# Performance work log

Hardware: AMD Instinct MI355X
Metric: run time of the kernel (lower is better)

The kernel has to match this reference:

```python
import jax, jax.numpy as jnp
import numpy as np

N_NODES = 40000
N_EDGES = 640000
N_FEAT = 128
HIDDEN = 128
N_GRAPHS = 64


def _sage_conv(x, src, dst, Wl, b, Wr):
    # PyG SAGEConv (aggr='mean', root_weight=True, normalize=False):
    # out_i = W_l @ mean_{j in N(i)} x_j + b + W_r @ x_i
    msg = x[src]                                             # [E, F]
    s = jax.ops.segment_sum(msg, dst, num_segments=N_NODES)  # [N, F]
    deg = jax.ops.segment_sum(jnp.ones((src.shape[0],), x.dtype), dst,
                              num_segments=N_NODES)
    agg = s / jnp.maximum(deg, 1.0)[:, None]
    return agg @ Wl + b + x @ Wr


def setup_inputs() -> dict:
    key = jax.random.key(0)
    ks = jax.random.split(key, 12)
    sc = 1.0 / np.sqrt(N_FEAT)
    x = jax.random.normal(ks[0], (N_NODES, N_FEAT), dtype=jnp.float32)
    edge_index = jax.random.randint(ks[1], (2, N_EDGES), 0, N_NODES, dtype=jnp.int32)
    batch = jnp.sort(jax.random.randint(ks[2], (N_NODES,), 0, N_GRAPHS, dtype=jnp.int32))
    mk = lambda k, shp: (jax.random.normal(k, shp, dtype=jnp.float32) * sc)
    return {
        'x': x, 'edge_index': edge_index, 'batch': batch,
        'W1l': mk(ks[3], (N_FEAT, HIDDEN)), 'b1': jnp.zeros((HIDDEN,), jnp.float32),
        'W1r': mk(ks[4], (N_FEAT, HIDDEN)),
        'W2l': mk(ks[5], (HIDDEN, HIDDEN)), 'b2': jnp.zeros((HIDDEN,), jnp.float32),
        'W2r': mk(ks[6], (HIDDEN, HIDDEN)),
        'W3l': mk(ks[7], (HIDDEN, HIDDEN)), 'b3': jnp.zeros((HIDDEN,), jnp.float32),
        'W3r': mk(ks[8], (HIDDEN, HIDDEN)),
        'Wlin': mk(ks[9], (3 * HIDDEN, HIDDEN)), 'blin': jnp.zeros((HIDDEN,), jnp.float32),
    }


def reference(x, edge_index, batch, W1l, b1, W1r, W2l, b2, W2r, W3l, b3, W3r, Wlin, blin):
    src, dst = edge_index[0], edge_index[1]
    h1 = jax.nn.relu(_sage_conv(x, src, dst, W1l, b1, W1r))
    h2 = jax.nn.relu(_sage_conv(h1, src, dst, W2l, b2, W2r))
    h3 = jax.nn.relu(_sage_conv(h2, src, dst, W3l, b3, W3r))
    h = jnp.concatenate([h1, h2, h3], axis=1)                # [N, 3*H]
    pooled = jax.ops.segment_sum(h, batch, num_segments=N_GRAPHS)  # global_add_pool
    out = jax.nn.relu(pooled @ Wlin + blin)                  # [G, H]
    return out
```

## Files before the change

### kernel.cpp

```cpp
#include <hip/hip_runtime.h>
#include <hip/hip_bf16.h>

#define N_NODES 40000
#define N_EDGES 640000
#define NFEAT 128
#define NGRAPHS 64
#define ECAP 768

typedef __attribute__((ext_vector_type(8))) short short8;
typedef __attribute__((ext_vector_type(4))) float float4v;

static __device__ __forceinline__ float bf2f(unsigned short u) {
    unsigned int x = ((unsigned int)u) << 16;
    return __builtin_bit_cast(float, x);
}
static __device__ __forceinline__ unsigned short f2bf(float f) {
    unsigned int x = __builtin_bit_cast(unsigned int, f);
    unsigned int r = x + 0x7fffu + ((x >> 16) & 1u);
    return (unsigned short)(r >> 16);
}

__global__ void k_prep(const int* __restrict__ dst, int* __restrict__ deg,
                       const int* __restrict__ batch, int* __restrict__ goff,
                       const float* __restrict__ x, unsigned short* __restrict__ h0,
                       const float* __restrict__ Wl0, const float* __restrict__ Wr0,
                       const float* __restrict__ Wl1, const float* __restrict__ Wr1,
                       const float* __restrict__ Wl2, const float* __restrict__ Wr2,
                       unsigned short* __restrict__ Wt, float* __restrict__ pooled) {
    int b = blockIdx.x;
    if (b < 2500) {
        int e = b * 256 + threadIdx.x;
        if (e < N_EDGES) atomicAdd(&deg[dst[e]], 1);
    } else if (b < 2657) {
        int i = (b - 2500) * 256 + threadIdx.x;
        if (i >= N_NODES) return;
        int b1 = batch[i];
        int b0 = (i == 0) ? -1 : batch[i - 1];
        for (int g = b0 + 1; g <= b1; ++g) goff[g] = i;
        if (i == N_NODES - 1)
            for (int g = b1 + 1; g <= NGRAPHS; ++g) goff[g] = N_NODES;
    } else if (b < 5157) {
        int i = (b - 2657) * 256 + threadIdx.x;
        const int n = N_NODES * NFEAT / 8;
        if (i < n) {
            const float4* xf = (const float4*)x;
            float4 p0 = xf[2 * i], p1 = xf[2 * i + 1];
            uint4 v;
            v.x = (unsigned int)f2bf(p0.x) | ((unsigned int)f2bf(p0.y) << 16);
            v.y = (unsigned int)f2bf(p0.z) | ((unsigned int)f2bf(p0.w) << 16);
            v.z = (unsigned int)f2bf(p1.x) | ((unsigned int)f2bf(p1.y) << 16);
            v.w = (unsigned int)f2bf(p1.z) | ((unsigned int)f2bf(p1.w) << 16);
            ((uint4*)h0)[i] = v;
        }
    } else if (b < 5541) {
        int id = (b - 5157) * 256 + threadIdx.x;
        if (id >= 3 * 128 * 256) return;
        int l   = id >> 15;
        int rem = id & 32767;
        int nn  = rem >> 8;
        int k   = rem & 255;
        const float* Wl = (l == 0) ? Wl0 : (l == 1) ? Wl1 : Wl2;
        const float* Wr = (l == 0) ? Wr0 : (l == 1) ? Wr1 : Wr2;
        float v = (k < 128) ? Wl[k * 128 + nn] : Wr[(k - 128) * 128 + nn];
        Wt[id] = f2bf(v);
    } else {
        int j = (b - 5541) * 256 + threadIdx.x;
        if (j < NGRAPHS * 384) pooled[j] = 0.f;
    }
}

__global__ __launch_bounds__(1024) void k_scan(const int* __restrict__ deg,
                                               int* __restrict__ offsets,
                                               int* __restrict__ cursor) {
    __shared__ int ws[16];
    __shared__ int s_boff;
    int tid = threadIdx.x;
    int b = blockIdx.x;
    int lane = tid & 63, wave = tid >> 6;

    int lim = b << 10;
    int s = 0;
    for (int i = tid; i < lim; i += 1024) s += deg[i];
    for (int d = 1; d < 64; d <<= 1) s += __shfl_xor(s, d, 64);
    if (lane == 0) ws[wave] = s;
    __syncthreads();
    if (tid == 0) {
        int t = 0;
        for (int w = 0; w < 16; ++w) t += ws[w];
        s_boff = t;
    }
    __syncthreads();
    int boff = s_boff;

    int i = (b << 10) + tid;
    int v = (i < N_NODES) ? deg[i] : 0;
    int incl = v;
    for (int d = 1; d < 64; d <<= 1) {
        int t = __shfl_up(incl, d, 64);
        if (lane >= d) incl += t;
    }
    __syncthreads();
    if (lane == 63) ws[wave] = incl;
    __syncthreads();
    if (wave == 0 && lane < 16) {
        int w = ws[lane];
        for (int d = 1; d < 16; d <<= 1) {
            int t = __shfl_up(w, d, 64);
            if (lane >= d) w += t;
        }
        ws[lane] = w;
    }
    __syncthreads();
    int waveOff = (wave == 0) ? 0 : ws[wave - 1];
    if (i < N_NODES) {
        int o = boff + waveOff + incl - v;
        offsets[i] = o;
        cursor[i]  = o;
    }
    if (b == 39 && tid == 0) offsets[N_NODES] = N_EDGES;
}

__global__ void k_fill(const int* __restrict__ src, const int* __restrict__ dst,
                       int* __restrict__ cursor, int* __restrict__ esrc) {
    int e = blockIdx.x * 256 + threadIdx.x;
    if (e < N_EDGES) {
        int d = dst[e];
        int p = atomicAdd(&cursor[d], 1);
        esrc[p] = src[e];
    }
}

__global__ __launch_bounds__(256, 8) void k_sage(
        const unsigned short* __restrict__ hin,
        const int* __restrict__ offsets,
        const int* __restrict__ esrc,
        const int* __restrict__ batch,
        const unsigned short* __restrict__ Wt,
        const float* __restrict__ bias,
        unsigned short* __restrict__ hout,
        float* __restrict__ poolseg) {
    __shared__ __align__(16) unsigned short As[32][264];
    __shared__ int eidx[ECAP];
    int tid = threadIdx.x;
    int row0 = blockIdx.x * 32;

    int estart = offsets[row0];
    int ecnt   = offsets[row0 + 32] - estart;
    int staged = ecnt < ECAP ? ecnt : ECAP;

    for (int p = 0; p < 2; ++p) {
        int ci = tid + p * 256;
        int r = ci >> 4, c8 = ci & 15;
        uint4 v = *(const uint4*)(hin + (size_t)(row0 + r) * 128 + c8 * 8);
        *(uint4*)(&As[r][128 + c8 * 8]) = v;
    }
    for (int t = tid; t < staged; t += 256) eidx[t] = esrc[estart + t];
    __syncthreads();

    {
        int grp = tid >> 4;
        int sub = tid & 15;
        for (int nn = 0; nn < 2; ++nn) {
            int r = nn * 16 + grp;
            int node = row0 + r;
            int beg = offsets[node], end = offsets[node + 1];
            float a[8];
            for (int i = 0; i < 8; ++i) a[i] = 0.f;
            auto acc8 = [&](uint4 u) {
                a[0] += bf2f((unsigned short)(u.x & 0xffffu));
                a[1] += bf2f((unsigned short)(u.x >> 16));
                a[2] += bf2f((unsigned short)(u.y & 0xffffu));
                a[3] += bf2f((unsigned short)(u.y >> 16));
                a[4] += bf2f((unsigned short)(u.z & 0xffffu));
                a[5] += bf2f((unsigned short)(u.z >> 16));
                a[6] += bf2f((unsigned short)(u.w & 0xffffu));
                a[7] += bf2f((unsigned short)(u.w >> 16));
            };
            if (end - estart <= staged) {
                int lj = beg - estart, lend = end - estart;
                for (; lj + 8 <= lend; lj += 8) {
                    int s0 = eidx[lj],     s1 = eidx[lj + 1];
                    int s2 = eidx[lj + 2], s3 = eidx[lj + 3];
                    int s4 = eidx[lj + 4], s5 = eidx[lj + 5];
                    int s6 = eidx[lj + 6], s7 = eidx[lj + 7];
                    uint4 u0 = *(const uint4*)(hin + (size_t)s0 * 128 + sub * 8);
                    uint4 u1 = *(const uint4*)(hin + (size_t)s1 * 128 + sub * 8);
                    uint4 u2 = *(const uint4*)(hin + (size_t)s2 * 128 + sub * 8);
                    uint4 u3 = *(const uint4*)(hin + (size_t)s3 * 128 + sub * 8);
                    uint4 u4 = *(const uint4*)(hin + (size_t)s4 * 128 + sub * 8);
                    uint4 u5 = *(const uint4*)(hin + (size_t)s5 * 128 + sub * 8);
                    uint4 u6 = *(const uint4*)(hin + (size_t)s6 * 128 + sub * 8);
                    uint4 u7 = *(const uint4*)(hin + (size_t)s7 * 128 + sub * 8);
                    acc8(u0); acc8(u1); acc8(u2); acc8(u3);
                    acc8(u4); acc8(u5); acc8(u6); acc8(u7);
                }
                for (; lj < lend; ++lj) {
                    int s = eidx[lj];
                    uint4 u = *(const uint4*)(hin + (size_t)s * 128 + sub * 8);
                    acc8(u);
                }
            } else {
                for (int j = beg; j < end; ++j) {
                    int s = esrc[j];
                    uint4 u = *(const uint4*)(hin + (size_t)s * 128 + sub * 8);
                    acc8(u);
                }
            }
            int deg = end - beg;
            float inv = 1.f / (float)(deg > 1 ? deg : 1);
            uint4 v;
            v.x = (unsigned int)f2bf(a[0] * inv) | ((unsigned int)f2bf(a[1] * inv) << 16);
            v.y = (unsigned int)f2bf(a[2] * inv) | ((unsigned int)f2bf(a[3] * inv) << 16);
            v.z = (unsigned int)f2bf(a[4] * inv) | ((unsigned int)f2bf(a[5] * inv) << 16);
            v.w = (unsigned int)f2bf(a[6] * inv) | ((unsigned int)f2bf(a[7] * inv) << 16);
            *(uint4*)(&As[r][sub * 8]) = v;
        }
    }
    __syncthreads();

    int wave = tid >> 6, lane = tid & 63;
    int quad = lane >> 4, l16 = lane & 15;
    float4v acc[2][2];
    for (int rt = 0; rt < 2; ++rt)
        for (int ct = 0; ct < 2; ++ct) acc[rt][ct] = {0.f, 0.f, 0.f, 0.f};

    int ncol0 = wave * 32;
    for (int kc = 0; kc < 8; ++kc) {
        int k0 = kc * 32 + quad * 8;
        short8 a[2], b[2];
        for (int rt = 0; rt < 2; ++rt)
            a[rt] = *(const short8*)(&As[rt * 16 + l16][k0]);
        for (int ct = 0; ct < 2; ++ct)
            b[ct] = *(const short8*)(Wt + (size_t)(ncol0 + ct * 16 + l16) * 256 + k0);
        for (int rt = 0; rt < 2; ++rt)
            for (int ct = 0; ct < 2; ++ct)
                acc[rt][ct] = __builtin_amdgcn_mfma_f32_16x16x32_bf16(
                    a[rt], b[ct], acc[rt][ct], 0, 0, 0);
    }

    __syncthreads();
    float* Ps = (float*)&As[0][0];
    int* sbatch = eidx;
    if (tid < 32) sbatch[tid] = batch[row0 + tid];

    for (int ct = 0; ct < 2; ++ct) {
        int col = ncol0 + ct * 16 + l16;
        float bv = bias[col];
        for (int rt = 0; rt < 2; ++rt) {
            int r0 = rt * 16 + quad * 4;
            for (int i = 0; i < 4; ++i) {
                float v = acc[rt][ct][i] + bv;
                v = v > 0.f ? v : 0.f;
                if (hout) hout[(size_t)(row0 + r0 + i) * 128 + col] = f2bf(v);
                Ps[(r0 + i) * 132 + col] = v;
            }
        }
    }
    __syncthreads();

    {
        int half = tid >> 7;
        int c = tid & 127;
        int rbase = half * 16;
        float accp = 0.f;
        int cur = sbatch[rbase];
        for (int r = rbase; r < rbase + 16; ++r) {
            int g = sbatch[r];
            if (g != cur) {
                atomicAdd(&poolseg[cur * 384 + c], accp);
                accp = 0.f;
                cur = g;
            }
            accp += Ps[r * 132 + c];
        }
        atomicAdd(&poolseg[cur * 384 + c], accp);
    }
}

__global__ void k_final(const float* __restrict__ pooled,
                        const float* __restrict__ Wlin,
                        const float* __restrict__ blin,
                        float* __restrict__ out) {
    int g = blockIdx.x, col = threadIdx.x;
    float acc = blin[col];
    for (int k = 0; k < 384; ++k)
        acc = fmaf(pooled[g * 384 + k], Wlin[k * 128 + col], acc);
    out[g * 128 + col] = acc > 0.f ? acc : 0.f;
}

extern "C" void kernel_launch(void* const* d_in, const int* in_sizes, int n_in,
                              void* d_out, int out_size, void* d_ws, size_t ws_size,
                              hipStream_t stream) {
    const float* x    = (const float*)d_in[0];
    const int*   ei   = (const int*)d_in[1];
    const int*   src  = ei;
    const int*   dst  = ei + N_EDGES;
    const int*   batch = (const int*)d_in[2];
    const float* W1l = (const float*)d_in[3];
    const float* b1  = (const float*)d_in[4];
    const float* W1r = (const float*)d_in[5];
    const float* W2l = (const float*)d_in[6];
    const float* b2  = (const float*)d_in[7];
    const float* W2r = (const float*)d_in[8];
    const float* W3l = (const float*)d_in[9];
    const float* b3  = (const float*)d_in[10];
    const float* W3r = (const float*)d_in[11];
    const float* Wlin = (const float*)d_in[12];
    const float* blin = (const float*)d_in[13];
    float* out = (float*)d_out;

    char* ws = (char*)d_ws;
    size_t off = 0;
    auto alloc = [&](size_t bytes) -> char* {
        char* p = ws + off;
        off = (off + bytes + 255) & ~(size_t)255;
        return p;
    };
    int* offsets = (int*)alloc((N_NODES + 1) * sizeof(int));
    int* cursor  = (int*)alloc(N_NODES * sizeof(int));
    int* deg     = (int*)alloc(N_NODES * sizeof(int));
    int* goff    = (int*)alloc((NGRAPHS + 1) * sizeof(int));
    int* esrc    = (int*)alloc(N_EDGES * sizeof(int));
    unsigned short* h0   = (unsigned short*)alloc((size_t)N_NODES * 128 * 2);
    unsigned short* h1   = (unsigned short*)alloc((size_t)N_NODES * 128 * 2);
    unsigned short* h2   = (unsigned short*)alloc((size_t)N_NODES * 128 * 2);
    unsigned short* Wt   = (unsigned short*)alloc(3 * 256 * 128 * 2);
    float* pooled = (float*)alloc(NGRAPHS * 384 * sizeof(float));

    hipMemsetAsync(deg, 0, N_NODES * sizeof(int), stream);

    k_prep<<<5637, 256, 0, stream>>>(dst, deg, batch, goff, x, h0,
                                     W1l, W1r, W2l, W2r, W3l, W3r, Wt, pooled);
    k_scan<<<40, 1024, 0, stream>>>(deg, offsets, cursor);
    k_fill<<<(N_EDGES + 255) / 256, 256, 0, stream>>>(src, dst, cursor, esrc);

    k_sage<<<1250, 256, 0, stream>>>(h0, offsets, esrc, batch, Wt,
                                     b1, h1, pooled);
    k_sage<<<1250, 256, 0, stream>>>(h1, offsets, esrc, batch, Wt + 32768,
                                     b2, h2, pooled + 128);
    k_sage<<<1250, 256, 0, stream>>>(h2, offsets, esrc, batch, Wt + 2 * 32768,
                                     b3, (unsigned short*)nullptr, pooled + 256);

    k_final<<<NGRAPHS, 128, 0, stream>>>(pooled, Wlin, blin, out);
}
```

Baseline: 264.7 us.

## Store CSR source indices as 16-bit, pack bf16 accumulation, split final matvec

Stores the CSR source-index array as unsigned short instead of int, which halves index traffic in the fill and gather phases and lets ECAP grow to 1024 within the same shared footprint. Rewrites the bf16-to-float accumulation as float2 vector adds with mask/shift unpacking, which may map to packed FP32 adds. Splits the final 384-long dot product across two thread halves and combines them through shared memory. Node IDs go up to 40000, which fits in 16 bits, but the truncation only holds while N_NODES stays below 65536.

```diff
diff --git a/kernel.cpp b/kernel.cpp
--- a/kernel.cpp
+++ b/kernel.cpp
@@ -5,10 +5,11 @@
 #define N_EDGES 640000
 #define NFEAT 128
 #define NGRAPHS 64
-#define ECAP 768
+#define ECAP 1024
 
 typedef __attribute__((ext_vector_type(8))) short short8;
 typedef __attribute__((ext_vector_type(4))) float float4v;
+typedef __attribute__((ext_vector_type(2))) float float2v;
 
 static __device__ __forceinline__ float bf2f(unsigned short u) {
     unsigned int x = ((unsigned int)u) << 16;
@@ -121,26 +122,26 @@
 }
 
 __global__ void k_fill(const int* __restrict__ src, const int* __restrict__ dst,
-                       int* __restrict__ cursor, int* __restrict__ esrc) {
+                       int* __restrict__ cursor, unsigned short* __restrict__ esrc) {
     int e = blockIdx.x * 256 + threadIdx.x;
     if (e < N_EDGES) {
         int d = dst[e];
         int p = atomicAdd(&cursor[d], 1);
-        esrc[p] = src[e];
+        esrc[p] = (unsigned short)src[e];
     }
 }
 
 __global__ __launch_bounds__(256, 8) void k_sage(
         const unsigned short* __restrict__ hin,
         const int* __restrict__ offsets,
-        const int* __restrict__ esrc,
+        const unsigned short* __restrict__ esrc,
         const int* __restrict__ batch,
         const unsigned short* __restrict__ Wt,
         const float* __restrict__ bias,
         unsigned short* __restrict__ hout,
         float* __restrict__ poolseg) {
     __shared__ __align__(16) unsigned short As[32][264];
-    __shared__ int eidx[ECAP];
+    __shared__ __align__(16) unsigned short eidx[ECAP];
     int tid = threadIdx.x;
     int row0 = blockIdx.x * 32;
 
@@ -164,17 +165,18 @@
             int r = nn * 16 + grp;
             int node = row0 + r;
             int beg = offsets[node], end = offsets[node + 1];
-            float a[8];
-            for (int i = 0; i < 8; ++i) a[i] = 0.f;
+            float2v a0 = {0.f, 0.f}, a1 = a0, a2 = a0, a3 = a0;
             auto acc8 = [&](uint4 u) {
-                a[0] += bf2f((unsigned short)(u.x & 0xffffu));
-                a[1] += bf2f((unsigned short)(u.x >> 16));
-                a[2] += bf2f((unsigned short)(u.y & 0xffffu));
-                a[3] += bf2f((unsigned short)(u.y >> 16));
-                a[4] += bf2f((unsigned short)(u.z & 0xffffu));
-                a[5] += bf2f((unsigned short)(u.z >> 16));
-                a[6] += bf2f((unsigned short)(u.w & 0xffffu));
-                a[7] += bf2f((unsigned short)(u.w >> 16));
+                float2v t0, t1, t2, t3;
+                t0.x = __builtin_bit_cast(float, u.x << 16);
+                t0.y = __builtin_bit_cast(float, u.x & 0xffff0000u);
+                t1.x = __builtin_bit_cast(float, u.y << 16);
+                t1.y = __builtin_bit_cast(float, u.y & 0xffff0000u);
+                t2.x = __builtin_bit_cast(float, u.z << 16);
+                t2.y = __builtin_bit_cast(float, u.z & 0xffff0000u);
+                t3.x = __builtin_bit_cast(float, u.w << 16);
+                t3.y = __builtin_bit_cast(float, u.w & 0xffff0000u);
+                a0 += t0; a1 += t1; a2 += t2; a3 += t3;
             };
             if (end - estart <= staged) {
                 int lj = beg - estart, lend = end - estart;
@@ -209,10 +211,10 @@
             int deg = end - beg;
             float inv = 1.f / (float)(deg > 1 ? deg : 1);
             uint4 v;
-            v.x = (unsigned int)f2bf(a[0] * inv) | ((unsigned int)f2bf(a[1] * inv) << 16);
-            v.y = (unsigned int)f2bf(a[2] * inv) | ((unsigned int)f2bf(a[3] * inv) << 16);
-            v.z = (unsigned int)f2bf(a[4] * inv) | ((unsigned int)f2bf(a[5] * inv) << 16);
-            v.w = (unsigned int)f2bf(a[6] * inv) | ((unsigned int)f2bf(a[7] * inv) << 16);
+            v.x = (unsigned int)f2bf(a0.x * inv) | ((unsigned int)f2bf(a0.y * inv) << 16);
+            v.y = (unsigned int)f2bf(a1.x * inv) | ((unsigned int)f2bf(a1.y * inv) << 16);
+            v.z = (unsigned int)f2bf(a2.x * inv) | ((unsigned int)f2bf(a2.y * inv) << 16);
+            v.w = (unsigned int)f2bf(a3.x * inv) | ((unsigned int)f2bf(a3.y * inv) << 16);
             *(uint4*)(&As[r][sub * 8]) = v;
         }
     }
@@ -240,7 +242,7 @@
 
     __syncthreads();
     float* Ps = (float*)&As[0][0];
-    int* sbatch = eidx;
+    int* sbatch = (int*)&eidx[0];
     if (tid < 32) sbatch[tid] = batch[row0 + tid];
 
     for (int ct = 0; ct < 2; ++ct) {
@@ -281,11 +283,20 @@
                         const float* __restrict__ Wlin,
                         const float* __restrict__ blin,
                         float* __restrict__ out) {
-    int g = blockIdx.x, col = threadIdx.x;
-    float acc = blin[col];
-    for (int k = 0; k < 384; ++k)
+    __shared__ float part[128];
+    int g = blockIdx.x;
+    int t = threadIdx.x;
+    int col = t & 127, half = t >> 7;
+    int k0 = half * 192;
+    float acc = 0.f;
+    for (int k = k0; k < k0 + 192; ++k)
         acc = fmaf(pooled[g * 384 + k], Wlin[k * 128 + col], acc);
-    out[g * 128 + col] = acc > 0.f ? acc : 0.f;
+    if (half) part[col] = acc;
+    __syncthreads();
+    if (!half) {
+        float v = acc + part[col] + blin[col];
+        out[g * 128 + col] = v > 0.f ? v : 0.f;
+    }
 }
 
 extern "C" void kernel_launch(void* const* d_in, const int* in_sizes, int n_in,
@@ -320,7 +331,7 @@
     int* cursor  = (int*)alloc(N_NODES * sizeof(int));
     int* deg     = (int*)alloc(N_NODES * sizeof(int));
     int* goff    = (int*)alloc((NGRAPHS + 1) * sizeof(int));
-    int* esrc    = (int*)alloc(N_EDGES * sizeof(int));
+    unsigned short* esrc = (unsigned short*)alloc(N_EDGES * sizeof(unsigned short));
     unsigned short* h0   = (unsigned short*)alloc((size_t)N_NODES * 128 * 2);
     unsigned short* h1   = (unsigned short*)alloc((size_t)N_NODES * 128 * 2);
     unsigned short* h2   = (unsigned short*)alloc((size_t)N_NODES * 128 * 2);
@@ -341,5 +352,5 @@
     k_sage<<<1250, 256, 0, stream>>>(h2, offsets, esrc, batch, Wt + 2 * 32768,
                                      b3, (unsigned short*)nullptr, pooled + 256);
 
-    k_final<<<NGRAPHS, 128, 0, stream>>>(pooled, Wlin, blin, out);
-}
+    k_final<<<NGRAPHS, 256, 0, stream>>>(pooled, Wlin, blin, out);
+}
```

Result: faster. 255.9 us (-3.3%).
